# Optimization experiments

Measured on AMD Instinct MI355X. Metric: run time of the kernel, lower is better.

## Reference

```python
import jax, jax.numpy as jnp
import numpy as np

B, C, H, W = 4, 256, 64, 64
CQ = C // 8


def setup_inputs() -> dict:
    key = jax.random.key(0)
    ks = jax.random.split(key, 7)
    x = jax.random.normal(ks[0], (B, C, H, W), dtype=jnp.float32)
    Wq = jax.random.normal(ks[1], (CQ, C), dtype=jnp.float32) * 0.02
    bq = jnp.zeros((CQ,), dtype=jnp.float32)
    Wk = jax.random.normal(ks[2], (CQ, C), dtype=jnp.float32) * 0.02
    bk = jnp.zeros((CQ,), dtype=jnp.float32)
    Wv = jax.random.normal(ks[3], (C, C), dtype=jnp.float32) * 0.02
    bv = jnp.zeros((C,), dtype=jnp.float32)
    return {"x": x, "Wq": Wq, "bq": bq, "Wk": Wk, "bk": bk, "Wv": Wv, "bv": bv}


def reference(x, Wq, bq, Wk, bk, Wv, bv):
    b, c, h, w = x.shape
    n = h * w
    xf = x.reshape(b, c, n)                                   # [B,C,N]
    # 1x1 convs are per-pixel GEMMs
    q = jnp.einsum('qc,bcn->bnq', Wq, xf) + bq                # [B,N,Cq]
    k = jnp.einsum('qc,bcn->bqn', Wk, xf) + bk[None, :, None] # [B,Cq,N]
    v = jnp.einsum('vc,bcn->bnv', Wv, xf) + bv                # [B,N,C]
    scale = float(n) ** 0.5
    energy = jnp.einsum('bnq,bqm->bnm', q, k) / scale         # [B,N,N]
    attn = jax.nn.softmax(energy, axis=-1)
    out = jnp.einsum('bnm,bmv->bnv', attn, v)                 # [B,N,C]
    # Faithful to torch's out.view(B,C,H,W) applied to the contiguous [B,N,C]
    # tensor: a raw memory reinterpretation, NOT a transpose.
    return out.reshape(b, c, h, w)
```

## Files before the change

kernel.cpp:

```cpp
#include <hip/hip_runtime.h>

#define BATCH 4
#define CH    256
#define NPIX  4096
#define CQD   32

typedef __bf16 bf16;
typedef bf16 bf16x8 __attribute__((ext_vector_type(8)));
typedef bf16 bf16x4 __attribute__((ext_vector_type(4)));
typedef float f32x4 __attribute__((ext_vector_type(4)));
typedef float f32x16 __attribute__((ext_vector_type(16)));

#define MFMA16 __builtin_amdgcn_mfma_f32_16x16x32_bf16
#define MFMA32 __builtin_amdgcn_mfma_f32_32x32x16_bf16

#define GLOAD_LDS16(g, l) __builtin_amdgcn_global_load_lds( \
    (const __attribute__((address_space(1))) void*)(g),     \
    (__attribute__((address_space(3))) void*)(l), 16, 0, 0)

__global__ __launch_bounds__(256) void prep_kernel(
    const float* __restrict__ Wq, const float* __restrict__ bq,
    const float* __restrict__ Wk, const float* __restrict__ bk,
    const float* __restrict__ Wv, const float* __restrict__ bv,
    bf16* __restrict__ Wb, float* __restrict__ bb)
{
    int r = blockIdx.x, c = threadIdx.x;
    const float* W; const float* bs; float sc; int rr;
    if (r < 32)      { W = Wq; bs = bq; sc = 0.015625f * 1.44269504088896340736f; rr = r; }
    else if (r < 64) { W = Wk; bs = bk; sc = 1.0f;      rr = r - 32; }
    else             { W = Wv; bs = bv; sc = 1.0f;      rr = r - 64; }
    Wb[(size_t)r * CH + c] = (bf16)(W[(size_t)rr * CH + c] * sc);
    if (c == 0) bb[r] = bs[rr] * sc;
}

__global__ __launch_bounds__(256) void proj_kernel(
    const float* __restrict__ x,
    const bf16* __restrict__ Wb, const float* __restrict__ bb,
    bf16* __restrict__ qp, bf16* __restrict__ kp, bf16* __restrict__ vT)
{
    __shared__ __align__(16) bf16 xT[32][264];
    __shared__ __align__(16) bf16 vstage[4][16][40];

    const int t  = threadIdx.x;
    const int b  = blockIdx.x >> 7;
    const int n0 = (blockIdx.x & 127) << 5;
    const int w    = t >> 6;
    const int lane = t & 63;
    const int l16  = t & 15;
    const int quad = (t & 63) >> 4;

    const float* xb = x + (size_t)b * CH * NPIX;
#pragma unroll
    for (int j = 0; j < 8; ++j) {
        int id = t + j * 256;
        int c  = id >> 3;
        int n4 = (id & 7) << 2;
        float4 vv = *(const float4*)(xb + (size_t)c * NPIX + n0 + n4);
        xT[n4 + 0][c] = (bf16)vv.x;
        xT[n4 + 1][c] = (bf16)vv.y;
        xT[n4 + 2][c] = (bf16)vv.z;
        xT[n4 + 3][c] = (bf16)vv.w;
    }
    __syncthreads();

    for (int rt = 0; rt < 5; ++rt) {
        int ro = w * 80 + rt * 16;
        int kind = (ro < 32) ? 0 : (ro < 64) ? 1 : 2;

        bf16x8 afrag[8];
        const bf16* wrow = Wb + (size_t)(ro + l16) * CH + quad * 8;
#pragma unroll
        for (int kc = 0; kc < 8; ++kc)
            afrag[kc] = *(const bf16x8*)(wrow + kc * 32);
        float bv4[4];
#pragma unroll
        for (int r = 0; r < 4; ++r) bv4[r] = bb[ro + quad * 4 + r];

#pragma unroll
        for (int nt = 0; nt < 2; ++nt) {
            f32x4 acc = {0.f, 0.f, 0.f, 0.f};
#pragma unroll
            for (int kc = 0; kc < 8; ++kc) {
                bf16x8 bfr = *(const bf16x8*)&xT[nt * 16 + l16][kc * 32 + quad * 8];
                acc = MFMA16(afrag[kc], bfr, acc, 0, 0, 0);
            }
            if (kind != 2) {
                bf16x4 pk;
#pragma unroll
                for (int r = 0; r < 4; ++r)
                    pk[r] = (bf16)(acc[r] + bv4[r]);
                int n = n0 + nt * 16 + l16;
                int col = (kind == 0 ? ro : ro - 32) + quad * 4;
                bf16* dst = (kind == 0) ? qp : kp;
                *(bf16x4*)&dst[((size_t)b * NPIX + n) * CQD + col] = pk;
            } else {
#pragma unroll
                for (int r = 0; r < 4; ++r)
                    vstage[w][quad * 4 + r][nt * 16 + l16] = (bf16)(acc[r] + bv4[r]);
            }
        }
        if (kind == 2) {
            int vrow = lane >> 2, vcc = lane & 3;
            bf16x8 chunk = *(const bf16x8*)&vstage[w][vrow][vcc * 8];
            *(bf16x8*)&vT[((size_t)b * CH + (ro - 64) + vrow) * NPIX + n0 + vcc * 8] = chunk;
        }
    }
}

template<int S, bool DIRECT>
__global__ __launch_bounds__(256, 2) void attn_kernel(
    const bf16* __restrict__ qp, const bf16* __restrict__ kp,
    const bf16* __restrict__ vT,
    bf16* __restrict__ Opart, float* __restrict__ Lpart,
    float* __restrict__ out)
{
    __shared__ __align__(16) bf16 Vt[2][256][64];
    __shared__ __align__(16) bf16 PbS[128][64];

    const int t    = threadIdx.x;
    const int bid  = blockIdx.x;
    const int s    = bid % S;
    const int tq   = bid / S;
    const int b    = tq >> 5;
    const int qt   = tq & 31;
    const int n0   = qt << 7;
    const int w    = t >> 6;
    const int lane = t & 63;
    const int l16  = t & 15;
    const int quad = (t & 63) >> 4;
    const int sw   = l16 & 7;
    const int l32  = lane & 31;
    const int h    = lane >> 5;
    const int qh   = w >> 1;
    const int chb  = (w & 1) * 128;

    const bf16* qpb = qp + ((size_t)b * NPIX + n0 + w * 32) * CQD;
    bf16x8 qfrag[2];
    qfrag[0] = *(const bf16x8*)(qpb + (size_t)l16 * CQD + quad * 8);
    qfrag[1] = *(const bf16x8*)(qpb + (size_t)(16 + l16) * CQD + quad * 8);

    f32x16 o[2][4];
#pragma unroll
    for (int i = 0; i < 2; ++i)
#pragma unroll
        for (int j = 0; j < 4; ++j)
#pragma unroll
            for (int r = 0; r < 16; ++r) o[i][j][r] = 0.f;
    float lsum[2] = {0.f, 0.f};

    const bf16* kpb = kp + (size_t)b * NPIX * CQD;
    const bf16* vTb = vT + (size_t)b * CH * NPIX;
    const int k0 = s * (NPIX / S);
    const int iters = NPIX / S / 64;

    const int vrow_off = lane >> 3;
    const int vchunk   = (lane & 7) ^ vrow_off;
    auto issue_vt = [&](int buf, int m0) {
#pragma unroll
        for (int j = 0; j < 8; ++j) {
            int rowbase = j * 32 + w * 8;
            const bf16* src = vTb + (size_t)(rowbase + vrow_off) * NPIX + m0 + vchunk * 8;
            GLOAD_LDS16(src, &Vt[buf][rowbase][0]);
        }
    };
    auto load_kf = [&](int m0, bf16x8* kf) {
#pragma unroll
        for (int mt = 0; mt < 4; ++mt)
            kf[mt] = *(const bf16x8*)(kpb + (size_t)(m0 + mt * 16 + l16) * CQD + quad * 8);
    };

    bf16x8 kfa[4], kfb[4];
    issue_vt(0, k0);
    load_kf(k0, kfa);
    __syncthreads();

    for (int mi = 0; mi < iters; ++mi) {
        const int cur = mi & 1;
        const int m0  = k0 + (mi << 6);
        if (mi + 1 < iters) {
            issue_vt(cur ^ 1, m0 + 64);
            load_kf(m0 + 64, kfb);
        }

        f32x4 sv[2][4];
#pragma unroll
        for (int mt = 0; mt < 4; ++mt) {
            f32x4 z = {0.f, 0.f, 0.f, 0.f};
            sv[0][mt] = MFMA16(kfa[mt], qfrag[0], z, 0, 0, 0);
            sv[1][mt] = MFMA16(kfa[mt], qfrag[1], z, 0, 0, 0);
        }

#pragma unroll
        for (int g = 0; g < 2; ++g) {
            float rs = 0.f;
#pragma unroll
            for (int mt = 0; mt < 4; ++mt) {
                bf16x4 pk;
#pragma unroll
                for (int r = 0; r < 4; ++r) {
                    float e = exp2f(sv[g][mt][r]);
                    rs += e;
                    pk[r] = (bf16)e;
                }
                int slot = (2 * mt + (quad >> 1)) ^ sw;
                *(bf16x4*)&PbS[w * 32 + g * 16 + l16][slot * 8 + (quad & 1) * 4] = pk;
            }
            lsum[g] += rs;
        }
        __syncthreads();

        bf16x8 pA[2][4];
#pragma unroll
        for (int t32 = 0; t32 < 2; ++t32)
#pragma unroll
            for (int kg = 0; kg < 4; ++kg) {
                int row = qh * 64 + t32 * 32 + l32;
                pA[t32][kg] = *(const bf16x8*)&PbS[row][((2 * kg + h) ^ (l32 & 7)) * 8];
            }
#pragma unroll
        for (int ct = 0; ct < 4; ++ct) {
            int vrow = chb + ct * 32 + l32;
            bf16x8 vB[4];
#pragma unroll
            for (int kg = 0; kg < 4; ++kg)
                vB[kg] = *(const bf16x8*)&Vt[cur][vrow][((2 * kg + h) ^ (l32 & 7)) * 8];
#pragma unroll
            for (int t32 = 0; t32 < 2; ++t32)
#pragma unroll
                for (int kg = 0; kg < 4; ++kg)
                    o[t32][ct] = MFMA32(pA[t32][kg], vB[kg], o[t32][ct], 0, 0, 0);
        }
        __syncthreads();
#pragma unroll
        for (int i = 0; i < 4; ++i) kfa[i] = kfb[i];
    }

    float l_g[2];
#pragma unroll
    for (int g = 0; g < 2; ++g) {
        float v = lsum[g];
        v += __shfl_xor(v, 16);
        v += __shfl_xor(v, 32);
        l_g[g] = v;
    }
    float* lsh = (float*)PbS;
    if (quad == 0) {
#pragma unroll
        for (int g = 0; g < 2; ++g)
            lsh[w * 32 + g * 16 + l16] = l_g[g];
    }
    __syncthreads();

    const size_t prb2 = ((size_t)s * BATCH + b) * NPIX + n0;
    if (!DIRECT && quad == 0) {
#pragma unroll
        for (int g = 0; g < 2; ++g)
            Lpart[prb2 + w * 32 + g * 16 + l16] = l_g[g];
    }

    bf16* eb = (bf16*)Vt + (size_t)w * 32 * 136;
#pragma unroll
    for (int t32 = 0; t32 < 2; ++t32) {
        float rinv[16];
#pragma unroll
        for (int reg = 0; reg < 16; ++reg) {
            int q_r = (reg & 3) + 8 * (reg >> 2) + 4 * h;
            rinv[reg] = 1.0f / lsh[qh * 64 + t32 * 32 + q_r];
        }
        if (!DIRECT) {
#pragma unroll
            for (int ct = 0; ct < 4; ++ct)
#pragma unroll
                for (int reg = 0; reg < 16; ++reg) {
                    int q_r = (reg & 3) + 8 * (reg >> 2) + 4 * h;
                    eb[q_r * 136 + ct * 32 + l32] = (bf16)(o[t32][ct][reg] * rinv[reg]);
                }
            int vrow = lane >> 4, vcc = lane & 15;
#pragma unroll
            for (int p = 0; p < 8; ++p) {
                int row = p * 4 + vrow;
                bf16x8 chunk = *(const bf16x8*)&eb[row * 136 + vcc * 8];
                *(bf16x8*)&Opart[(prb2 + qh * 64 + t32 * 32 + row) * CH +
                                 chb + vcc * 8] = chunk;
            }
        } else {
            float* ob = out + (prb2 + qh * 64 + t32 * 32) * CH + chb;
#pragma unroll
            for (int ct = 0; ct < 4; ++ct)
#pragma unroll
                for (int reg = 0; reg < 16; ++reg) {
                    int q_r = (reg & 3) + 8 * (reg >> 2) + 4 * h;
                    ob[(size_t)q_r * CH + ct * 32 + l32] = o[t32][ct][reg] * rinv[reg];
                }
        }
    }
}

template<int S>
__global__ __launch_bounds__(256) void combine_kernel(
    const bf16* __restrict__ Opart, const float* __restrict__ Lpart,
    float* __restrict__ out)
{
    int idx  = blockIdx.x * 256 + threadIdx.x;
    int nrow = idx >> 4;
    int cc   = (idx & 15) * 16;
    int b    = nrow >> 12, nin = nrow & 4095;

    size_t pr[S];
    float  ls[S], wsum = 0.f;
#pragma unroll
    for (int s = 0; s < S; ++s) {
        pr[s] = ((size_t)s * BATCH + b) * NPIX + nin;
        ls[s] = Lpart[pr[s]];
        wsum += ls[s];
    }
    float inv = 1.0f / wsum;

    bf16x8 ov[S][2];
#pragma unroll
    for (int s = 0; s < S; ++s) {
        ov[s][0] = *(const bf16x8*)&Opart[pr[s] * CH + cc];
        ov[s][1] = *(const bf16x8*)&Opart[pr[s] * CH + cc + 8];
    }

    float acc[16];
#pragma unroll
    for (int j = 0; j < 16; ++j) acc[j] = 0.f;
#pragma unroll
    for (int s = 0; s < S; ++s) {
        float wn = ls[s] * inv;
#pragma unroll
        for (int k = 0; k < 2; ++k)
#pragma unroll
            for (int j = 0; j < 8; ++j)
                acc[k * 8 + j] += wn * (float)ov[s][k][j];
    }
#pragma unroll
    for (int k = 0; k < 4; ++k) {
        float4 o4 = {acc[4 * k], acc[4 * k + 1], acc[4 * k + 2], acc[4 * k + 3]};
        *(float4*)&out[(size_t)nrow * CH + cc + 4 * k] = o4;
    }
}

extern "C" void kernel_launch(void* const* d_in, const int* in_sizes, int n_in,
                              void* d_out, int out_size, void* d_ws, size_t ws_size,
                              hipStream_t stream) {
    const float* x  = (const float*)d_in[0];
    const float* Wq = (const float*)d_in[1];
    const float* bq = (const float*)d_in[2];
    const float* Wk = (const float*)d_in[3];
    const float* bk = (const float*)d_in[4];
    const float* Wv = (const float*)d_in[5];
    const float* bv = (const float*)d_in[6];
    float* out = (float*)d_out;

    char* ws = (char*)d_ws;
    const size_t qpB   = (size_t)BATCH * NPIX * CQD * 2;
    const size_t vTB   = (size_t)BATCH * CH * NPIX * 2;
    const size_t WbB   = (size_t)320 * CH * 2;
    const size_t bbB   = 320 * 4 + 768;
    const size_t baseB = 2 * qpB + vTB + WbB + bbB;
    const size_t oprtB = (size_t)BATCH * NPIX * CH * 2;
    const size_t mlB   = (size_t)BATCH * NPIX * 4;

    bf16*  qp = (bf16*)ws;
    bf16*  kp = (bf16*)(ws + qpB);
    bf16*  vT = (bf16*)(ws + 2 * qpB);
    bf16*  Wb = (bf16*)(ws + 2 * qpB + vTB);
    float* bb = (float*)(ws + 2 * qpB + vTB + WbB);

    prep_kernel<<<dim3(320), dim3(256), 0, stream>>>(Wq, bq, Wk, bk, Wv, bv, Wb, bb);
    proj_kernel<<<dim3(BATCH * (NPIX / 32)), dim3(256), 0, stream>>>(
        x, Wb, bb, qp, kp, vT);

    auto need = [&](int S) { return baseB + (size_t)S * (oprtB + mlB); };
    int S = (ws_size >= need(4)) ? 4 : (ws_size >= need(2)) ? 2
          : (ws_size >= need(1)) ? 1 : 0;

    if (S > 0) {
        bf16*  Opart = (bf16*)(ws + baseB);
        float* Lpart = (float*)(ws + baseB + (size_t)S * oprtB);
        if (S == 4) {
            attn_kernel<4, false><<<dim3(128 * 4), dim3(256), 0, stream>>>(
                qp, kp, vT, Opart, Lpart, out);
            combine_kernel<4><<<dim3(1024), dim3(256), 0, stream>>>(Opart, Lpart, out);
        } else if (S == 2) {
            attn_kernel<2, false><<<dim3(128 * 2), dim3(256), 0, stream>>>(
                qp, kp, vT, Opart, Lpart, out);
            combine_kernel<2><<<dim3(1024), dim3(256), 0, stream>>>(Opart, Lpart, out);
        } else {
            attn_kernel<1, false><<<dim3(128), dim3(256), 0, stream>>>(
                qp, kp, vT, Opart, Lpart, out);
            combine_kernel<1><<<dim3(1024), dim3(256), 0, stream>>>(Opart, Lpart, out);
        }
    } else {
        attn_kernel<1, true><<<dim3(128), dim3(256), 0, stream>>>(
            qp, kp, vT, nullptr, nullptr, out);
    }
}
```

Before: 145.2 us.

## Fuse split-K combine into attention kernel via last-block atomic counter

```diff
diff --git a/kernel.cpp b/kernel.cpp
--- a/kernel.cpp
+++ b/kernel.cpp
@@ -17,6 +17,16 @@
 #define GLOAD_LDS16(g, l) __builtin_amdgcn_global_load_lds( \
     (const __attribute__((address_space(1))) void*)(g),     \
     (__attribute__((address_space(3))) void*)(l), 16, 0, 0)
+
+__device__ __forceinline__ float fast_exp2(float x) {
+#if __has_builtin(__builtin_amdgcn_exp2f)
+    return __builtin_amdgcn_exp2f(x);
+#else
+    float r;
+    asm("v_exp_f32 %0, %1" : "=v"(r) : "v"(x));
+    return r;
+#endif
+}
 
 __global__ __launch_bounds__(256) void prep_kernel(
     const float* __restrict__ Wq, const float* __restrict__ bq,
@@ -112,6 +122,7 @@
     const bf16* __restrict__ qp, const bf16* __restrict__ kp,
     const bf16* __restrict__ vT,
     bf16* __restrict__ Opart, float* __restrict__ Lpart,
+    int* __restrict__ cnt,
     float* __restrict__ out)
 {
     __shared__ __align__(16) bf16 Vt[2][256][64];
@@ -198,7 +209,7 @@
                 bf16x4 pk;
 #pragma unroll
                 for (int r = 0; r < 4; ++r) {
-                    float e = exp2f(sv[g][mt][r]);
+                    float e = fast_exp2(sv[g][mt][r]);
                     rs += e;
                     pk[r] = (bf16)e;
                 }
@@ -294,51 +305,57 @@
                 }
         }
     }
-}
-
-template<int S>
-__global__ __launch_bounds__(256) void combine_kernel(
-    const bf16* __restrict__ Opart, const float* __restrict__ Lpart,
-    float* __restrict__ out)
-{
-    int idx  = blockIdx.x * 256 + threadIdx.x;
-    int nrow = idx >> 4;
-    int cc   = (idx & 15) * 16;
-    int b    = nrow >> 12, nin = nrow & 4095;
-
-    size_t pr[S];
-    float  ls[S], wsum = 0.f;
-#pragma unroll
-    for (int s = 0; s < S; ++s) {
-        pr[s] = ((size_t)s * BATCH + b) * NPIX + nin;
-        ls[s] = Lpart[pr[s]];
-        wsum += ls[s];
-    }
-    float inv = 1.0f / wsum;
-
-    bf16x8 ov[S][2];
-#pragma unroll
-    for (int s = 0; s < S; ++s) {
-        ov[s][0] = *(const bf16x8*)&Opart[pr[s] * CH + cc];
-        ov[s][1] = *(const bf16x8*)&Opart[pr[s] * CH + cc + 8];
-    }
-
-    float acc[16];
-#pragma unroll
-    for (int j = 0; j < 16; ++j) acc[j] = 0.f;
-#pragma unroll
-    for (int s = 0; s < S; ++s) {
-        float wn = ls[s] * inv;
-#pragma unroll
-        for (int k = 0; k < 2; ++k)
-#pragma unroll
-            for (int j = 0; j < 8; ++j)
-                acc[k * 8 + j] += wn * (float)ov[s][k][j];
-    }
-#pragma unroll
-    for (int k = 0; k < 4; ++k) {
-        float4 o4 = {acc[4 * k], acc[4 * k + 1], acc[4 * k + 2], acc[4 * k + 3]};
-        *(float4*)&out[(size_t)nrow * CH + cc + 4 * k] = o4;
+
+    if (!DIRECT) {
+        __syncthreads();
+        __threadfence();
+        volatile int* flag = (volatile int*)((int*)PbS + 192);
+        if (t == 0)
+            *flag = atomicAdd(&cnt[b * 32 + qt], 1);
+        __syncthreads();
+        if (*flag == S - 1) {
+            __threadfence();
+#pragma unroll
+            for (int it = 0; it < 8; ++it) {
+                int li = it * 256 + t;
+                int r  = li >> 4;
+                int cc = (li & 15) * 16;
+                size_t rb = (size_t)b * NPIX + n0 + r;
+                float ls2[S], wsum = 0.f;
+#pragma unroll
+                for (int sp = 0; sp < S; ++sp) {
+                    ls2[sp] = Lpart[(size_t)sp * BATCH * NPIX + rb];
+                    wsum += ls2[sp];
+                }
+                float inv2 = 1.0f / wsum;
+                bf16x8 ovv[S][2];
+#pragma unroll
+                for (int sp = 0; sp < S; ++sp) {
+                    const bf16* op = Opart + ((size_t)sp * BATCH * NPIX + rb) * CH + cc;
+                    ovv[sp][0] = *(const bf16x8*)op;
+                    ovv[sp][1] = *(const bf16x8*)(op + 8);
+                }
+                float acc2[16];
+#pragma unroll
+                for (int j = 0; j < 16; ++j) acc2[j] = 0.f;
+#pragma unroll
+                for (int sp = 0; sp < S; ++sp) {
+                    float wn = ls2[sp] * inv2;
+#pragma unroll
+                    for (int k2 = 0; k2 < 2; ++k2)
+#pragma unroll
+                        for (int j = 0; j < 8; ++j)
+                            acc2[k2 * 8 + j] += wn * (float)ovv[sp][k2][j];
+                }
+                float* ob2 = out + rb * CH + cc;
+#pragma unroll
+                for (int k2 = 0; k2 < 4; ++k2) {
+                    float4 o4 = {acc2[4 * k2], acc2[4 * k2 + 1],
+                                 acc2[4 * k2 + 2], acc2[4 * k2 + 3]};
+                    *(float4*)&ob2[4 * k2] = o4;
+                }
+            }
+        }
     }
 }
 
@@ -362,6 +379,7 @@
     const size_t baseB = 2 * qpB + vTB + WbB + bbB;
     const size_t oprtB = (size_t)BATCH * NPIX * CH * 2;
     const size_t mlB   = (size_t)BATCH * NPIX * 4;
+    const size_t cntB  = 1024;
 
     bf16*  qp = (bf16*)ws;
     bf16*  kp = (bf16*)(ws + qpB);
@@ -369,32 +387,31 @@
     bf16*  Wb = (bf16*)(ws + 2 * qpB + vTB);
     float* bb = (float*)(ws + 2 * qpB + vTB + WbB);
 
+    auto need = [&](int S) { return baseB + (size_t)S * (oprtB + mlB) + cntB; };
+    int S = (ws_size >= need(4)) ? 4 : (ws_size >= need(2)) ? 2
+          : (ws_size >= need(1)) ? 1 : 0;
+
     prep_kernel<<<dim3(320), dim3(256), 0, stream>>>(Wq, bq, Wk, bk, Wv, bv, Wb, bb);
     proj_kernel<<<dim3(BATCH * (NPIX / 32)), dim3(256), 0, stream>>>(
         x, Wb, bb, qp, kp, vT);
 
-    auto need = [&](int S) { return baseB + (size_t)S * (oprtB + mlB); };
-    int S = (ws_size >= need(4)) ? 4 : (ws_size >= need(2)) ? 2
-          : (ws_size >= need(1)) ? 1 : 0;
-
     if (S > 0) {
         bf16*  Opart = (bf16*)(ws + baseB);
         float* Lpart = (float*)(ws + baseB + (size_t)S * oprtB);
+        int*   cnt   = (int*)(ws + baseB + (size_t)S * (oprtB + mlB));
+        hipMemsetAsync((void*)cnt, 0, 128 * sizeof(int), stream);
         if (S == 4) {
             attn_kernel<4, false><<<dim3(128 * 4), dim3(256), 0, stream>>>(
-                qp, kp, vT, Opart, Lpart, out);
-            combine_kernel<4><<<dim3(1024), dim3(256), 0, stream>>>(Opart, Lpart, out);
+                qp, kp, vT, Opart, Lpart, cnt, out);
         } else if (S == 2) {
             attn_kernel<2, false><<<dim3(128 * 2), dim3(256), 0, stream>>>(
-                qp, kp, vT, Opart, Lpart, out);
-            combine_kernel<2><<<dim3(1024), dim3(256), 0, stream>>>(Opart, Lpart, out);
+                qp, kp, vT, Opart, Lpart, cnt, out);
         } else {
             attn_kernel<1, false><<<dim3(128), dim3(256), 0, stream>>>(
-                qp, kp, vT, Opart, Lpart, out);
-            combine_kernel<1><<<dim3(1024), dim3(256), 0, stream>>>(Opart, Lpart, out);
+                qp, kp, vT, Opart, Lpart, cnt, out);
         }
     } else {
         attn_kernel<1, true><<<dim3(128), dim3(256), 0, stream>>>(
-            qp, kp, vT, nullptr, nullptr, out);
+            qp, kp, vT, nullptr, nullptr, nullptr, out);
     }
 }
```

Measured after the change: 229.7 us. 1.58x slower.
